# Kernel tuning notes

Measured on AMD Instinct MI355X. Metric: run time of the kernel, lower is better.

Reference implementation:

```python
import jax, jax.numpy as jnp
import numpy as np

SEQ, B, IN_DIM, EMB, HID, L = 2048, 32, 512, 256, 256, 16
START, STOP = 0, 1
HH = HID // 2  # per-direction hidden size
NEG = -10000.0


def _lstm_dir(xs, Wih, Whh, b, h0, c0, reverse):
    # xs: (T, B, EMB); Wih: (4*HH, EMB); Whh: (4*HH, HH); b: (4*HH,)
    def step(carry, x):
        h, c = carry
        g = x @ Wih.T + h @ Whh.T + b  # (B, 4*HH)
        i, f, gg, o = jnp.split(g, 4, axis=-1)  # PyTorch gate order i,f,g,o
        c = jax.nn.sigmoid(f) * c + jax.nn.sigmoid(i) * jnp.tanh(gg)
        h = jax.nn.sigmoid(o) * jnp.tanh(c)
        return (h, c), h
    _, hs = jax.lax.scan(step, (h0, c0), xs, reverse=reverse)
    return hs  # (T, B, HH)


def _features(source_seq, in_W, in_b, Wih_f, Whh_f, b_f, Wih_b, Whh_b, b_b,
              out_W, out_b, h0, c0):
    x = source_seq @ in_W.T + in_b  # (T, B, EMB)
    hf = _lstm_dir(x, Wih_f, Whh_f, b_f, h0[0], c0[0], reverse=False)
    hb = _lstm_dir(x, Wih_b, Whh_b, b_b, h0[1], c0[1], reverse=True)
    h = jnp.concatenate([hf, hb], axis=-1)  # (T, B, HID)
    return h @ out_W.T + out_b  # (T, B, L)


def _viterbi(feats, transitions):
    # transitions[i, j]: score of transitioning to label i from label j
    fv = jnp.full((B, L), NEG, feats.dtype).at[:, START].set(0.0)

    def step(fv, feat):
        scores = fv[:, None, :] + transitions[None, :, :]  # (B, next, prev)
        bp = jnp.argmax(scores, axis=2).astype(jnp.int32)   # (B, L)
        fv = jnp.max(scores, axis=2) + feat
        return fv, bp

    fv, bps = jax.lax.scan(step, fv, feats)  # bps: (T, B, L)
    term = fv + transitions[STOP][None, :]   # (B, L)
    score = jnp.max(term, axis=1)            # (B,)
    best_last = jnp.argmax(term, axis=1).astype(jnp.int32)  # (B,)

    def back(lbl, bp):
        prev = jnp.take_along_axis(bp, lbl[:, None], axis=1)[:, 0]
        return prev, lbl

    _, path = jax.lax.scan(back, best_last, bps, reverse=True)  # (T, B)
    return score, path


def setup_inputs() -> dict:
    key = jax.random.key(0)
    ks = jax.random.split(key, 16)
    s = 0.05
    return {
        "source_seq": jax.random.normal(ks[0], (SEQ, B, IN_DIM), jnp.float32),
        "in_W": jax.random.normal(ks[1], (EMB, IN_DIM), jnp.float32) * s,
        "in_b": jnp.zeros((EMB,), jnp.float32),
        "Wih_f": jax.random.normal(ks[2], (4 * HH, EMB), jnp.float32) * s,
        "Whh_f": jax.random.normal(ks[3], (4 * HH, HH), jnp.float32) * s,
        "b_f": jnp.zeros((4 * HH,), jnp.float32),
        "Wih_b": jax.random.normal(ks[4], (4 * HH, EMB), jnp.float32) * s,
        "Whh_b": jax.random.normal(ks[5], (4 * HH, HH), jnp.float32) * s,
        "b_b": jnp.zeros((4 * HH,), jnp.float32),
        "out_W": jax.random.normal(ks[6], (L, HID), jnp.float32) * s,
        "out_b": jnp.zeros((L,), jnp.float32),
        "transitions": jax.random.normal(ks[7], (L, L), jnp.float32),
        "h0": jax.random.normal(ks[8], (2, B, HH), jnp.float32),
        "c0": jax.random.normal(ks[9], (2, B, HH), jnp.float32),
    }


def reference(source_seq, in_W, in_b, Wih_f, Whh_f, b_f, Wih_b, Whh_b, b_b,
              out_W, out_b, transitions, h0, c0):
    feats = _features(source_seq, in_W, in_b, Wih_f, Whh_f, b_f,
                      Wih_b, Whh_b, b_b, out_W, out_b, h0, c0)
    score, labels = _viterbi(feats, transitions)
    return score, labels
```

## Files before the change

### kernel.cpp

```cpp
#include <hip/hip_runtime.h>
#include <hip/hip_bf16.h>

typedef __attribute__((ext_vector_type(8))) short bf16x8;
typedef __attribute__((ext_vector_type(4))) float f32x4;
typedef __attribute__((ext_vector_type(4))) unsigned u32x4;
typedef __attribute__((ext_vector_type(2))) unsigned u32x2;

#define SEQT 2048
#define BATCH 32
#define INDIM 512
#define EMB 256
#define HHX 128
#define LBL 16
#define LOG2E 1.44269504f

__device__ __forceinline__ unsigned short f2bf(float f) {
    unsigned u = __float_as_uint(f);
    u += 0x7FFFu + ((u >> 16) & 1u);
    return (unsigned short)(u >> 16);
}
#define BLO(u) __uint_as_float((u) << 16)
#define BHI(u) __uint_as_float((u) & 0xffff0000u)

__device__ __forceinline__ float cell(float ig, float fg, float gg, float og, float& c) {
    float Ef = __builtin_amdgcn_exp2f(fminf(fg, 30.f));
    float Ei = __builtin_amdgcn_exp2f(fminf(ig, 30.f));
    float Eg = __builtin_amdgcn_exp2f(fminf(gg, 60.f));
    float Eo = __builtin_amdgcn_exp2f(fminf(og, 30.f));
    float pf = 1.f + Ef;
    float t1 = (Eg + 1.f) * (1.f + Ei);
    float num = c * t1 + (Eg - 1.f) * pf;
    float cn = num * __builtin_amdgcn_rcpf(pf * t1);
    c = cn;
    float E2 = __builtin_amdgcn_exp2f(fminf(2.f * LOG2E * cn, 60.f));
    float r3 = __builtin_amdgcn_rcpf((E2 + 1.f) * (1.f + Eo));
    return (E2 - 1.f) * r3;
}

__device__ __forceinline__ int orig_of(int gp) {
    return ((gp >> 4) & 3) * 128 + (gp >> 6) * 16 + (gp & 15);
}
__device__ __forceinline__ float gate_scale(int gp) {
    return (((gp >> 4) & 3) == 2) ? (2.f * LOG2E) : (-LOG2E);
}

__global__ __launch_bounds__(256) void k_prep_wc(
    const float* __restrict__ in_W, const float* __restrict__ in_b,
    const float* __restrict__ Wih_f, const float* __restrict__ b_f,
    const float* __restrict__ Wih_b, const float* __restrict__ b_b,
    unsigned short* __restrict__ Wc, float* __restrict__ bc)
{
    int G0 = blockIdx.x * 8;
    int tid = threadIdx.x;
    __shared__ float wrow[8][EMB];
    for (int e = tid; e < 8 * EMB; e += 256) {
        int r = e >> 8, ee = e & 255;
        int G = G0 + r, dir = G >> 9, gp = G & 511;
        wrow[r][ee] = (dir ? Wih_b : Wih_f)[orig_of(gp) * EMB + ee] * gate_scale(gp);
    }
    __syncthreads();
    for (int k = tid; k < INDIM; k += 256) {
        float acc[8] = {0, 0, 0, 0, 0, 0, 0, 0};
        #pragma unroll 4
        for (int e = 0; e < EMB; ++e) {
            float x = in_W[e * INDIM + k];
            #pragma unroll
            for (int r = 0; r < 8; ++r) acc[r] += wrow[r][e] * x;
        }
        #pragma unroll
        for (int r = 0; r < 8; ++r) Wc[(size_t)(G0 + r) * INDIM + k] = f2bf(acc[r]);
    }
    if (tid < 64) {
        for (int r = 0; r < 8; ++r) {
            float p = 0.f;
            for (int e = tid; e < EMB; e += 64) p += wrow[r][e] * in_b[e];
            for (int off = 32; off; off >>= 1) p += __shfl_xor(p, off);
            if (tid == 0) {
                int G = G0 + r, dir = G >> 9, gp = G & 511;
                bc[G] = (dir ? b_b : b_f)[orig_of(gp)] * gate_scale(gp) + p;
            }
        }
    }
}

__global__ __launch_bounds__(256) void k_prep_misc(
    const float* __restrict__ Whh_f, const float* __restrict__ Whh_b,
    const float* __restrict__ out_W,
    unsigned short* __restrict__ Whh_bf, unsigned short* __restrict__ outW_bf)
{
    int idx = blockIdx.x * 256 + threadIdx.x;
    int stride = gridDim.x * 256;
    for (int i = idx; i < 1024 * HHX; i += stride) {
        int G = i >> 7, k = i & 127;
        int dir = G >> 9, gp = G & 511;
        const float* Whh = dir ? Whh_b : Whh_f;
        Whh_bf[i] = f2bf(Whh[orig_of(gp) * HHX + k] * gate_scale(gp));
    }
    for (int i = idx; i < LBL * 256; i += stride) outW_bf[i] = f2bf(out_W[i]);
}

__global__ __launch_bounds__(512) void k_gemm_p(
    const float* __restrict__ S, const unsigned short* __restrict__ Wc,
    const float* __restrict__ bc, unsigned short* __restrict__ P2)
{
    int m0 = blockIdx.y * 64;
    int n0 = blockIdx.x * 256;
    int tid = threadIdx.x;
    int w = tid >> 6, l = tid & 63;
    int lr = l & 15, lq = l >> 4;
    int wm = w >> 2, wn = w & 3;

    __shared__ __align__(16) unsigned short Alds[64 * 64];
    __shared__ __align__(16) unsigned short Blds[256 * 64];

    const f32x4 fzero = {0.f, 0.f, 0.f, 0.f};
    f32x4 acc[2][4];
    #pragma unroll
    for (int a = 0; a < 2; ++a)
        #pragma unroll
        for (int b = 0; b < 4; ++b) acc[a][b] = fzero;

    for (int kt = 0; kt < 8; ++kt) {
        {
            int r = tid >> 3, c = tid & 7;
            const float* src = S + (size_t)(m0 + r) * INDIM + kt * 64 + c * 8;
            float4 v0 = *(const float4*)src;
            float4 v1 = *(const float4*)(src + 4);
            unsigned g0, g1, g2, g3;
            asm("v_cvt_pk_bf16_f32 %0, %1, %2" : "=v"(g0) : "v"(v0.x), "v"(v0.y));
            asm("v_cvt_pk_bf16_f32 %0, %1, %2" : "=v"(g1) : "v"(v0.z), "v"(v0.w));
            asm("v_cvt_pk_bf16_f32 %0, %1, %2" : "=v"(g2) : "v"(v1.x), "v"(v1.y));
            asm("v_cvt_pk_bf16_f32 %0, %1, %2" : "=v"(g3) : "v"(v1.z), "v"(v1.w));
            u32x4 wv = {g0, g1, g2, g3};
            *(u32x4*)((char*)Alds + r * 128 + ((c * 16) ^ ((r & 7) << 4))) = wv;
        }
        {
            int r = tid >> 1, h = tid & 1;
            const unsigned short* bs = Wc + (size_t)(n0 + r) * INDIM + kt * 64;
            #pragma unroll
            for (int cc = 0; cc < 4; ++cc) {
                int ch = h * 4 + cc;
                bf16x8 v = *(const bf16x8*)(bs + ch * 8);
                *(bf16x8*)((char*)Blds + r * 128 + ((ch * 16) ^ ((r & 7) << 4))) = v;
            }
        }
        __syncthreads();
        bf16x8 af[2][2], bfv[4][2];
        #pragma unroll
        for (int tm = 0; tm < 2; ++tm)
            #pragma unroll
            for (int kk = 0; kk < 2; ++kk) {
                int ra = wm * 32 + tm * 16 + lr;
                af[tm][kk] = *(const bf16x8*)((char*)Alds + ra * 128 + ((kk * 64 + lq * 16) ^ ((ra & 7) << 4)));
            }
        #pragma unroll
        for (int tn = 0; tn < 4; ++tn)
            #pragma unroll
            for (int kk = 0; kk < 2; ++kk) {
                int rb = wn * 64 + tn * 16 + lr;
                bfv[tn][kk] = *(const bf16x8*)((char*)Blds + rb * 128 + ((kk * 64 + lq * 16) ^ ((rb & 7) << 4)));
            }
        #pragma unroll
        for (int tm = 0; tm < 2; ++tm)
            #pragma unroll
            for (int tn = 0; tn < 4; ++tn)
                #pragma unroll
                for (int kk = 0; kk < 2; ++kk)
                    acc[tm][tn] = __builtin_amdgcn_mfma_f32_16x16x32_bf16(af[tm][kk], bfv[tn][kk], acc[tm][tn], 0, 0, 0);
        __syncthreads();
    }
    #pragma unroll
    for (int tn = 0; tn < 4; ++tn) {
        int n = n0 + wn * 64 + tn * 16 + lr;
        float bias = bc[n];
        int dir2 = n >> 9, nn = n & 511;
        int w2 = nn >> 6, q2 = (nn >> 4) & 3, lr2 = nn & 15;
        #pragma unroll
        for (int tm = 0; tm < 2; ++tm) {
            int t = blockIdx.y * 2 + wm;
            int bq2 = tm * 2 + (lq >> 1);
            int tid0 = w2 * 64 + (lq & 1) * 32 + lr2;
            size_t base = (((size_t)(t * 2 + dir2) * 4 + bq2) * 512 + tid0) * 8 + q2 * 2;
            float f0 = acc[tm][tn][0] + bias, f1 = acc[tm][tn][1] + bias;
            float f2 = acc[tm][tn][2] + bias, f3 = acc[tm][tn][3] + bias;
            unsigned p01, p23;
            asm("v_cvt_pk_bf16_f32 %0, %1, %2" : "=v"(p01) : "v"(f0), "v"(f1));
            asm("v_cvt_pk_bf16_f32 %0, %1, %2" : "=v"(p23) : "v"(f2), "v"(f3));
            *(unsigned*)(P2 + base) = p01;
            *(unsigned*)(P2 + base + 128) = p23;
        }
    }
}

__global__ __launch_bounds__(512) void k_lstm(
    const unsigned short* __restrict__ P2, const unsigned short* __restrict__ Whh_bf,
    const float* __restrict__ h0, const float* __restrict__ c0,
    unsigned short* __restrict__ H)
{
    int blk = blockIdx.x;
    int dir = blk >> 2, bq = blk & 3;
    int tid = threadIdx.x;
    int w = tid >> 6, l = tid & 63;
    int lr = l & 15, lq = l >> 4;

    __shared__ __align__(16) unsigned short hbuf[2][16 * 128];
    char* hb = (char*)hbuf;

    bf16x8 bfrag[4][4];
    #pragma unroll
    for (int q = 0; q < 4; ++q)
        #pragma unroll
        for (int ko = 0; ko < 4; ++ko) {
            int row = dir * 512 + w * 64 + q * 16 + lr;
            bfrag[q][ko] = *(const bf16x8*)(Whh_bf + (size_t)row * HHX + ko * 32 + lq * 8);
        }

    int u = w * 16 + lr;
    float cA = c0[(dir * 32 + bq * 8 + lq * 2) * HHX + u];
    float cB = c0[(dir * 32 + bq * 8 + lq * 2 + 1) * HHX + u];

    for (int e = tid; e < 2048; e += 512) {
        int r = e >> 7, uu = e & 127;
        unsigned short v = 0;
        if ((r & 3) < 2) {
            int b = (r >> 2) * 2 + (r & 3);
            v = f2bf(h0[(dir * 32 + bq * 8 + b) * HHX + uu]);
        }
        int addr = (r * 256 + uu * 2) ^ ((r & 7) << 4);
        *(unsigned short*)(hb + addr) = v;
        *(unsigned short*)(hb + 4096 + addr) = 0;
    }
    __syncthreads();

    const int rd0 = (lr * 256 + 0 * 64 + lq * 16) ^ ((lr & 7) << 4);
    const int rd1 = (lr * 256 + 1 * 64 + lq * 16) ^ ((lr & 7) << 4);
    const int rd2 = (lr * 256 + 2 * 64 + lq * 16) ^ ((lr & 7) << 4);
    const int rd3 = (lr * 256 + 3 * 64 + lq * 16) ^ ((lr & 7) << 4);
    const int rA = lq * 4, rB = lq * 4 + 1;
    const int waA = (rA * 256 + u * 2) ^ ((rA & 7) << 4);
    const int waB = (rB * 256 + u * 2) ^ ((rB & 7) << 4);

    int t0 = dir ? (SEQT - 1) : 0;
    const long long pstep = (dir ? -1LL : 1LL) * (2LL * 4 * 512 * 8);
    const unsigned short* pptr = P2 + (((size_t)(t0 * 2 + dir) * 4 + bq) * 512 + tid) * 8;
    bf16x8 pc = *(const bf16x8*)pptr;
    pptr += pstep;

    unsigned short* hpA = H + ((size_t)t0 * 32 + bq * 8 + lq * 2) * 256 + dir * 128 + u;
    const long long hstep = (dir ? -1LL : 1LL) * (32 * 256);

#define LBAR() asm volatile("s_waitcnt lgkmcnt(0)\n\ts_barrier" ::: "memory")

#define STEP(CUR, PF) do { \
    bf16x8 af0 = *(const bf16x8*)(hb + (CUR) * 4096 + rd0); \
    bf16x8 af1 = *(const bf16x8*)(hb + (CUR) * 4096 + rd1); \
    bf16x8 af2 = *(const bf16x8*)(hb + (CUR) * 4096 + rd2); \
    bf16x8 af3 = *(const bf16x8*)(hb + (CUR) * 4096 + rd3); \
    u32x4 u0 = __builtin_bit_cast(u32x4, pc); \
    if (PF) { pc = *(const bf16x8*)pptr; pptr += pstep; } \
    f32x4 a0 = {BLO(u0.x), BHI(u0.x), 0.f, 0.f}; \
    f32x4 a1 = {BLO(u0.y), BHI(u0.y), 0.f, 0.f}; \
    f32x4 a2 = {BLO(u0.z), BHI(u0.z), 0.f, 0.f}; \
    f32x4 a3 = {BLO(u0.w), BHI(u0.w), 0.f, 0.f}; \
    a0 = __builtin_amdgcn_mfma_f32_16x16x32_bf16(af0, bfrag[0][0], a0, 0, 0, 0); \
    a0 = __builtin_amdgcn_mfma_f32_16x16x32_bf16(af1, bfrag[0][1], a0, 0, 0, 0); \
    a0 = __builtin_amdgcn_mfma_f32_16x16x32_bf16(af2, bfrag[0][2], a0, 0, 0, 0); \
    a0 = __builtin_amdgcn_mfma_f32_16x16x32_bf16(af3, bfrag[0][3], a0, 0, 0, 0); \
    a1 = __builtin_amdgcn_mfma_f32_16x16x32_bf16(af0, bfrag[1][0], a1, 0, 0, 0); \
    a1 = __builtin_amdgcn_mfma_f32_16x16x32_bf16(af1, bfrag[1][1], a1, 0, 0, 0); \
    a1 = __builtin_amdgcn_mfma_f32_16x16x32_bf16(af2, bfrag[1][2], a1, 0, 0, 0); \
    a1 = __builtin_amdgcn_mfma_f32_16x16x32_bf16(af3, bfrag[1][3], a1, 0, 0, 0); \
    a2 = __builtin_amdgcn_mfma_f32_16x16x32_bf16(af0, bfrag[2][0], a2, 0, 0, 0); \
    a2 = __builtin_amdgcn_mfma_f32_16x16x32_bf16(af1, bfrag[2][1], a2, 0, 0, 0); \
    a2 = __builtin_amdgcn_mfma_f32_16x16x32_bf16(af2, bfrag[2][2], a2, 0, 0, 0); \
    a2 = __builtin_amdgcn_mfma_f32_16x16x32_bf16(af3, bfrag[2][3], a2, 0, 0, 0); \
    a3 = __builtin_amdgcn_mfma_f32_16x16x32_bf16(af0, bfrag[3][0], a3, 0, 0, 0); \
    a3 = __builtin_amdgcn_mfma_f32_16x16x32_bf16(af1, bfrag[3][1], a3, 0, 0, 0); \
    a3 = __builtin_amdgcn_mfma_f32_16x16x32_bf16(af2, bfrag[3][2], a3, 0, 0, 0); \
    a3 = __builtin_amdgcn_mfma_f32_16x16x32_bf16(af3, bfrag[3][3], a3, 0, 0, 0); \
    float hnA = cell(a0[0], a1[0], a2[0], a3[0], cA); \
    float hnB = cell(a0[1], a1[1], a2[1], a3[1], cB); \
    unsigned pk; \
    asm("v_cvt_pk_bf16_f32 %0, %1, %2" : "=v"(pk) : "v"(hnA), "v"(hnB)); \
    unsigned short sA = (unsigned short)pk, sB = (unsigned short)(pk >> 16); \
    char* wb = hb + (((CUR) ^ 1) * 4096); \
    *(unsigned short*)(wb + waA) = sA; \
    *(unsigned short*)(wb + waB) = sB; \
    hpA[0] = sA; hpA[256] = sB; \
    hpA += hstep; \
    LBAR(); \
} while (0)

    for (int it = 0; it < 1023; ++it) {
        STEP(0, true);
        STEP(1, true);
    }
    STEP(0, true);
    STEP(1, false);
#undef STEP
#undef LBAR
}

__global__ __launch_bounds__(256) void k_feats(
    const unsigned short* __restrict__ H, const unsigned short* __restrict__ outW_bf,
    const float* __restrict__ out_b, float* __restrict__ feats)
{
    int m0 = blockIdx.x * 64;
    int tid = threadIdx.x;
    int w = tid >> 6, l = tid & 63;
    int lr = l & 15, lq = l >> 4;
    __shared__ __align__(16) unsigned short Hl[64 * 256];

    {
        int r = tid >> 2, cb = (tid & 3) * 8;
        #pragma unroll
        for (int cc = 0; cc < 8; ++cc) {
            int c = cb + cc;
            bf16x8 v = *(const bf16x8*)(H + (size_t)(m0 + r) * 256 + c * 8);
            *(bf16x8*)((char*)Hl + r * 512 + ((c * 16) ^ ((r & 7) << 4))) = v;
        }
    }
    bf16x8 bw[8];
    #pragma unroll
    for (int ko = 0; ko < 8; ++ko)
        bw[ko] = *(const bf16x8*)(outW_bf + lr * 256 + ko * 32 + lq * 8);
    __syncthreads();
    int row = w * 16 + lr;
    f32x4 acc = {0.f, 0.f, 0.f, 0.f};
    #pragma unroll
    for (int ko = 0; ko < 8; ++ko) {
        bf16x8 a = *(const bf16x8*)((char*)Hl + row * 512 + ((ko * 64 + lq * 16) ^ ((row & 7) << 4)));
        acc = __builtin_amdgcn_mfma_f32_16x16x32_bf16(a, bw[ko], acc, 0, 0, 0);
    }
    float ob = out_b[lr];
    #pragma unroll
    for (int j = 0; j < 4; ++j) {
        int m = m0 + w * 16 + lq * 4 + j;
        feats[(size_t)m * 16 + lr] = acc[j] + ob;
    }
}

template <int CTRL>
__device__ __forceinline__ float dppf(float x) {
    return __int_as_float(__builtin_amdgcn_update_dpp(0, __float_as_int(x), CTRL, 0xF, 0xF, true));
}
template <int CTRL>
__device__ __forceinline__ int dppi(int x) {
    return __builtin_amdgcn_update_dpp(0, x, CTRL, 0xF, 0xF, true);
}

__global__ __launch_bounds__(64) void k_viterbi(
    const float* __restrict__ feats, const float* __restrict__ trans,
    float* __restrict__ out)
{
    int b = blockIdx.x;
    int l = threadIdx.x;
    int i = l >> 2, s = l & 3;
    __shared__ unsigned char bp[SEQT * 16];
    __shared__ __align__(16) float fch[256 * 16];
    __shared__ unsigned long long bp64[SEQT];

    float tr[4];
    #pragma unroll
    for (int m = 0; m < 4; ++m) tr[m] = trans[i * 16 + s * 4 + m];
    float fvloc[4];
    #pragma unroll
    for (int m = 0; m < 4; ++m) fvloc[m] = (s * 4 + m == 0) ? 0.f : -10000.f;

    int ga[4];
    #pragma unroll
    for (int m = 0; m < 4; ++m) ga[m] = (16 * s + 4 * m) * 4;

    for (int t = 0; t < SEQT; ++t) {
        if ((t & 255) == 0) {
            __syncthreads();
            for (int k = l; k < 256; k += 64) {
                const float4* src = (const float4*)(feats + (size_t)((t + k) * 32 + b) * 16);
                float4 v0 = src[0], v1 = src[1], v2 = src[2], v3 = src[3];
                float4* dst = (float4*)(fch + k * 16);
                dst[0] = v0; dst[1] = v1; dst[2] = v2; dst[3] = v3;
            }
            __syncthreads();
        }
        float best = fvloc[0] + tr[0];
        int bj = s * 4;
        #pragma unroll
        for (int m = 1; m < 4; ++m) {
            float v = fvloc[m] + tr[m];
            if (v > best) { best = v; bj = s * 4 + m; }
        }
        {
            float ov = dppf<0xB1>(best); int oj = dppi<0xB1>(bj);
            bool take = (ov > best) || (ov == best && oj < bj);
            best = take ? ov : best; bj = take ? oj : bj;
        }
        {
            float ov = dppf<0x4E>(best); int oj = dppi<0x4E>(bj);
            bool take = (ov > best) || (ov == best && oj < bj);
            best = take ? ov : best; bj = take ? oj : bj;
        }
        float fvn = best + fch[(t & 255) * 16 + i];
        if (s == 0) bp[t * 16 + i] = (unsigned char)bj;
        #pragma unroll
        for (int m = 0; m < 4; ++m)
            fvloc[m] = __int_as_float(__builtin_amdgcn_ds_bpermute(ga[m], __float_as_int(fvn)));
    }
    float bestS = fvloc[0] + trans[16 + s * 4];
    int bl = s * 4;
    #pragma unroll
    for (int m = 1; m < 4; ++m) {
        float tv = fvloc[m] + trans[16 + s * 4 + m];
        if (tv > bestS) { bestS = tv; bl = s * 4 + m; }
    }
    {
        float ov = dppf<0xB1>(bestS); int oj = dppi<0xB1>(bl);
        bool take = (ov > bestS) || (ov == bestS && oj < bl);
        bestS = take ? ov : bestS; bl = take ? oj : bl;
    }
    {
        float ov = dppf<0x4E>(bestS); int oj = dppi<0x4E>(bl);
        bool take = (ov > bestS) || (ov == bestS && oj < bl);
        bestS = take ? ov : bestS; bl = take ? oj : bl;
    }
    __syncthreads();
    for (int t = l; t < SEQT; t += 64) {
        const uint4* p = (const uint4*)(bp + t * 16);
        uint4 u = *p;
        unsigned n0 = (u.x | (u.x >> 4)) & 0x00FF00FFu; n0 = (n0 | (n0 >> 8)) & 0xFFFFu;
        unsigned n1 = (u.y | (u.y >> 4)) & 0x00FF00FFu; n1 = (n1 | (n1 >> 8)) & 0xFFFFu;
        unsigned n2 = (u.z | (u.z >> 4)) & 0x00FF00FFu; n2 = (n2 | (n2 >> 8)) & 0xFFFFu;
        unsigned n3 = (u.w | (u.w >> 4)) & 0x00FF00FFu; n3 = (n3 | (n3 >> 8)) & 0xFFFFu;
        bp64[t] = (unsigned long long)n0 | ((unsigned long long)n1 << 16)
                | ((unsigned long long)n2 << 32) | ((unsigned long long)n3 << 48);
    }
    __syncthreads();
    if (l == 0) out[b] = bestS;
    int lbl = bl;
    #pragma unroll 8
    for (int t = SEQT - 1; t >= 0; --t) {
        if ((t & 63) == l) out[32 + (size_t)t * 32 + b] = (float)lbl;
        lbl = (int)((bp64[t] >> (lbl * 4)) & 15ull);
    }
}

extern "C" void kernel_launch(void* const* d_in, const int* in_sizes, int n_in,
                              void* d_out, int out_size, void* d_ws, size_t ws_size,
                              hipStream_t stream) {
    const float* source = (const float*)d_in[0];
    const float* in_W  = (const float*)d_in[1];
    const float* in_b  = (const float*)d_in[2];
    const float* Wih_f = (const float*)d_in[3];
    const float* Whh_f = (const float*)d_in[4];
    const float* b_f   = (const float*)d_in[5];
    const float* Wih_b = (const float*)d_in[6];
    const float* Whh_b = (const float*)d_in[7];
    const float* b_b   = (const float*)d_in[8];
    const float* out_W = (const float*)d_in[9];
    const float* out_b = (const float*)d_in[10];
    const float* trans = (const float*)d_in[11];
    const float* h0    = (const float*)d_in[12];
    const float* c0    = (const float*)d_in[13];
    float* out = (float*)d_out;

    char* ws = (char*)d_ws;
    unsigned short* P2      = (unsigned short*)(ws);
    unsigned short* H       = (unsigned short*)(ws + 134217728);
    float*          feats   = (float*)         (ws + 167772160);
    unsigned short* Wc      = (unsigned short*)(ws + 171966464);
    float*          bc      = (float*)         (ws + 173015040);
    unsigned short* Whh_bf  = (unsigned short*)(ws + 173019136);
    unsigned short* outW_bf = (unsigned short*)(ws + 173281280);

    hipLaunchKernelGGL(k_prep_wc, dim3(128), dim3(256), 0, stream,
                       in_W, in_b, Wih_f, b_f, Wih_b, b_b, Wc, bc);
    hipLaunchKernelGGL(k_prep_misc, dim3(256), dim3(256), 0, stream,
                       Whh_f, Whh_b, out_W, Whh_bf, outW_bf);
    hipLaunchKernelGGL(k_gemm_p, dim3(4, 1024), dim3(512), 0, stream,
                       source, Wc, bc, P2);
    hipLaunchKernelGGL(k_lstm, dim3(8), dim3(512), 0, stream,
                       P2, Whh_bf, h0, c0, H);
    hipLaunchKernelGGL(k_feats, dim3(1024), dim3(256), 0, stream,
                       H, outW_bf, out_b, feats);
    hipLaunchKernelGGL(k_viterbi, dim3(32), dim3(64), 0, stream,
                       feats, trans, out);
}
```

Baseline: 1.926 ms.

## Split LSTM recurrence over 16 blocks with four batch rows each

The recurrent LSTM kernel now runs 16 workgroups instead of 8, so each block handles 4 batch rows per direction instead of 8. Each lane computes one hidden cell instead of two, which shortens the per-step critical path of gate activation math. The input-projection GEMM writes P2 in a matching layout with 4 packed gates per entry, using scalar 16-bit stores. In exchange the MFMA tiles are more sparsely filled (4 of 16 rows used), and the GEMM epilogue does more, narrower global stores.

```diff
diff --git a/kernel.cpp b/kernel.cpp
--- a/kernel.cpp
+++ b/kernel.cpp
@@ -178,16 +178,17 @@
         #pragma unroll
         for (int tm = 0; tm < 2; ++tm) {
             int t = blockIdx.y * 2 + wm;
-            int bq2 = tm * 2 + (lq >> 1);
-            int tid0 = w2 * 64 + (lq & 1) * 32 + lr2;
-            size_t base = (((size_t)(t * 2 + dir2) * 4 + bq2) * 512 + tid0) * 8 + q2 * 2;
+            int bq2 = tm * 4 + lq;
+            size_t fr = ((size_t)(t * 2 + dir2) * 8 + bq2) * 512;
             float f0 = acc[tm][tn][0] + bias, f1 = acc[tm][tn][1] + bias;
             float f2 = acc[tm][tn][2] + bias, f3 = acc[tm][tn][3] + bias;
             unsigned p01, p23;
             asm("v_cvt_pk_bf16_f32 %0, %1, %2" : "=v"(p01) : "v"(f0), "v"(f1));
             asm("v_cvt_pk_bf16_f32 %0, %1, %2" : "=v"(p23) : "v"(f2), "v"(f3));
-            *(unsigned*)(P2 + base) = p01;
-            *(unsigned*)(P2 + base + 128) = p23;
+            P2[(fr + (w2 * 64 + 0 * 16 + lr2)) * 4 + q2] = (unsigned short)p01;
+            P2[(fr + (w2 * 64 + 1 * 16 + lr2)) * 4 + q2] = (unsigned short)(p01 >> 16);
+            P2[(fr + (w2 * 64 + 2 * 16 + lr2)) * 4 + q2] = (unsigned short)p23;
+            P2[(fr + (w2 * 64 + 3 * 16 + lr2)) * 4 + q2] = (unsigned short)(p23 >> 16);
         }
     }
 }
@@ -198,7 +199,7 @@
     unsigned short* __restrict__ H)
 {
     int blk = blockIdx.x;
-    int dir = blk >> 2, bq = blk & 3;
+    int dir = blk >> 3, bq = blk & 7;
     int tid = threadIdx.x;
     int w = tid >> 6, l = tid & 63;
     int lr = l & 15, lq = l >> 4;
@@ -216,15 +217,14 @@
         }
 
     int u = w * 16 + lr;
-    float cA = c0[(dir * 32 + bq * 8 + lq * 2) * HHX + u];
-    float cB = c0[(dir * 32 + bq * 8 + lq * 2 + 1) * HHX + u];
+    float cA = c0[(dir * 32 + bq * 4 + lq) * HHX + u];
 
     for (int e = tid; e < 2048; e += 512) {
         int r = e >> 7, uu = e & 127;
         unsigned short v = 0;
-        if ((r & 3) < 2) {
-            int b = (r >> 2) * 2 + (r & 3);
-            v = f2bf(h0[(dir * 32 + bq * 8 + b) * HHX + uu]);
+        if ((r & 3) == 0) {
+            int b = r >> 2;
+            v = f2bf(h0[(dir * 32 + bq * 4 + b) * HHX + uu]);
         }
         int addr = (r * 256 + uu * 2) ^ ((r & 7) << 4);
         *(unsigned short*)(hb + addr) = v;
@@ -236,17 +236,16 @@
     const int rd1 = (lr * 256 + 1 * 64 + lq * 16) ^ ((lr & 7) << 4);
     const int rd2 = (lr * 256 + 2 * 64 + lq * 16) ^ ((lr & 7) << 4);
     const int rd3 = (lr * 256 + 3 * 64 + lq * 16) ^ ((lr & 7) << 4);
-    const int rA = lq * 4, rB = lq * 4 + 1;
+    const int rA = lq * 4;
     const int waA = (rA * 256 + u * 2) ^ ((rA & 7) << 4);
-    const int waB = (rB * 256 + u * 2) ^ ((rB & 7) << 4);
 
     int t0 = dir ? (SEQT - 1) : 0;
-    const long long pstep = (dir ? -1LL : 1LL) * (2LL * 4 * 512 * 8);
-    const unsigned short* pptr = P2 + (((size_t)(t0 * 2 + dir) * 4 + bq) * 512 + tid) * 8;
-    bf16x8 pc = *(const bf16x8*)pptr;
+    const long long pstep = (dir ? -1LL : 1LL) * (2LL * 8 * 512 * 4);
+    const unsigned short* pptr = P2 + (((size_t)(t0 * 2 + dir) * 8 + bq) * 512 + tid) * 4;
+    u32x2 pc = *(const u32x2*)pptr;
     pptr += pstep;
 
-    unsigned short* hpA = H + ((size_t)t0 * 32 + bq * 8 + lq * 2) * 256 + dir * 128 + u;
+    unsigned short* hpA = H + ((size_t)t0 * 32 + bq * 4 + lq) * 256 + dir * 128 + u;
     const long long hstep = (dir ? -1LL : 1LL) * (32 * 256);
 
 #define LBAR() asm volatile("s_waitcnt lgkmcnt(0)\n\ts_barrier" ::: "memory")
@@ -256,12 +255,12 @@
     bf16x8 af1 = *(const bf16x8*)(hb + (CUR) * 4096 + rd1); \
     bf16x8 af2 = *(const bf16x8*)(hb + (CUR) * 4096 + rd2); \
     bf16x8 af3 = *(const bf16x8*)(hb + (CUR) * 4096 + rd3); \
-    u32x4 u0 = __builtin_bit_cast(u32x4, pc); \
-    if (PF) { pc = *(const bf16x8*)pptr; pptr += pstep; } \
-    f32x4 a0 = {BLO(u0.x), BHI(u0.x), 0.f, 0.f}; \
-    f32x4 a1 = {BLO(u0.y), BHI(u0.y), 0.f, 0.f}; \
-    f32x4 a2 = {BLO(u0.z), BHI(u0.z), 0.f, 0.f}; \
-    f32x4 a3 = {BLO(u0.w), BHI(u0.w), 0.f, 0.f}; \
+    u32x2 u0 = pc; \
+    if (PF) { pc = *(const u32x2*)pptr; pptr += pstep; } \
+    f32x4 a0 = {BLO(u0.x), 0.f, 0.f, 0.f}; \
+    f32x4 a1 = {BHI(u0.x), 0.f, 0.f, 0.f}; \
+    f32x4 a2 = {BLO(u0.y), 0.f, 0.f, 0.f}; \
+    f32x4 a3 = {BHI(u0.y), 0.f, 0.f, 0.f}; \
     a0 = __builtin_amdgcn_mfma_f32_16x16x32_bf16(af0, bfrag[0][0], a0, 0, 0, 0); \
     a0 = __builtin_amdgcn_mfma_f32_16x16x32_bf16(af1, bfrag[0][1], a0, 0, 0, 0); \
     a0 = __builtin_amdgcn_mfma_f32_16x16x32_bf16(af2, bfrag[0][2], a0, 0, 0, 0); \
@@ -279,14 +278,11 @@
     a3 = __builtin_amdgcn_mfma_f32_16x16x32_bf16(af2, bfrag[3][2], a3, 0, 0, 0); \
     a3 = __builtin_amdgcn_mfma_f32_16x16x32_bf16(af3, bfrag[3][3], a3, 0, 0, 0); \
     float hnA = cell(a0[0], a1[0], a2[0], a3[0], cA); \
-    float hnB = cell(a0[1], a1[1], a2[1], a3[1], cB); \
     unsigned pk; \
-    asm("v_cvt_pk_bf16_f32 %0, %1, %2" : "=v"(pk) : "v"(hnA), "v"(hnB)); \
-    unsigned short sA = (unsigned short)pk, sB = (unsigned short)(pk >> 16); \
-    char* wb = hb + (((CUR) ^ 1) * 4096); \
-    *(unsigned short*)(wb + waA) = sA; \
-    *(unsigned short*)(wb + waB) = sB; \
-    hpA[0] = sA; hpA[256] = sB; \
+    asm("v_cvt_pk_bf16_f32 %0, %1, %2" : "=v"(pk) : "v"(hnA), "v"(hnA)); \
+    unsigned short sA = (unsigned short)pk; \
+    *(unsigned short*)(hb + (((CUR) ^ 1) * 4096) + waA) = sA; \
+    hpA[0] = sA; \
     hpA += hstep; \
     LBAR(); \
 } while (0)
@@ -477,7 +473,7 @@
                        Whh_f, Whh_b, out_W, Whh_bf, outW_bf);
     hipLaunchKernelGGL(k_gemm_p, dim3(4, 1024), dim3(512), 0, stream,
                        source, Wc, bc, P2);
-    hipLaunchKernelGGL(k_lstm, dim3(8), dim3(512), 0, stream,
+    hipLaunchKernelGGL(k_lstm, dim3(16), dim3(512), 0, stream,
                        P2, Whh_bf, h0, c0, H);
     hipLaunchKernelGGL(k_feats, dim3(1024), dim3(256), 0, stream,
                        H, outW_bf, out_b, feats);
```

Measured after the change: 1.824 ms. 5.2% less time.
